# Optimization experiments

Hardware: AMD Instinct MI355X
Metric: run time of the kernel (lower is better)

The kernel has to match this reference:

```python
import jax, jax.numpy as jnp
import numpy as np

N_NODES = 50000
N_EDGES = 800000
IN_C, OUT_C, EDGE_F, HEADS, HID, FINAL = 8, 16, 8, 4, 64, 128
NEG_SLOPE = 0.2  # PyG GATConv default LeakyReLU slope


def setup_inputs() -> dict:
    key = jax.random.key(0)
    ks = jax.random.split(key, 12)
    s = 0.1
    return {
        "x": jax.random.normal(ks[0], (N_NODES, IN_C), jnp.float32),
        "edge_index": jax.random.randint(ks[1], (2, N_EDGES), 0, N_NODES, jnp.int64),
        "edge_attr": jax.random.normal(ks[2], (N_EDGES, EDGE_F), jnp.float32),
        # NNConv params: root weight, bias, edge-MLP Linear(EDGE_F -> IN_C*OUT_C)
        "ecc_root": jax.random.normal(ks[3], (IN_C, OUT_C), jnp.float32) * s,
        "ecc_bias": jnp.zeros((OUT_C,), jnp.float32),
        "mlp_w": jax.random.normal(ks[4], (EDGE_F, IN_C * OUT_C), jnp.float32) * s,
        "mlp_b": jnp.zeros((IN_C * OUT_C,), jnp.float32),
        # GATConv params
        "gat_lin": jax.random.normal(ks[5], (OUT_C, HEADS * HID), jnp.float32) * s,
        "att_src": jax.random.normal(ks[6], (HEADS, HID), jnp.float32) * s,
        "att_dst": jax.random.normal(ks[7], (HEADS, HID), jnp.float32) * s,
        "gat_bias": jnp.zeros((HEADS * HID,), jnp.float32),
        # final Linear
        "fc_w": jax.random.normal(ks[8], (HEADS * HID, FINAL), jnp.float32) * s,
        "fc_b": jnp.zeros((FINAL,), jnp.float32),
    }


def _forward(x, edge_index, edge_attr, ecc_root, ecc_bias, mlp_w, mlp_b,
             gat_lin, att_src, att_dst, gat_bias, fc_w, fc_b):
    src, dst = edge_index[0], edge_index[1]  # messages flow src -> dst

    # ---- NNConv (edge-conditioned conv), aggr='add' ----
    # per-edge weight matrices [E, IN_C, OUT_C] from edge MLP
    w_e = (edge_attr @ mlp_w + mlp_b).reshape(-1, IN_C, OUT_C)
    msg = jnp.einsum('ei,eio->eo', x[src], w_e)                 # [E, OUT_C]
    agg = jax.ops.segment_sum(msg, dst, num_segments=N_NODES)   # [N, OUT_C]
    h = jax.nn.relu(x @ ecc_root + agg + ecc_bias)              # [N, OUT_C]

    # ---- GATConv (heads concatenated) ----
    g = (h @ gat_lin).reshape(N_NODES, HEADS, HID)              # [N, H, D]
    a_src = jnp.einsum('nhd,hd->nh', g, att_src)                # [N, H]
    a_dst = jnp.einsum('nhd,hd->nh', g, att_dst)
    e = jax.nn.leaky_relu(a_src[src] + a_dst[dst], NEG_SLOPE)   # [E, H]
    # segment softmax over incoming edges of each dst node
    e_max = jax.ops.segment_max(e, dst, num_segments=N_NODES)   # [N, H]
    e_max = jnp.where(jnp.isfinite(e_max), e_max, 0.0)
    e_exp = jnp.exp(e - e_max[dst])                             # [E, H]
    denom = jax.ops.segment_sum(e_exp, dst, num_segments=N_NODES)
    alpha = e_exp / (denom[dst] + 1e-16)                        # [E, H]
    out = jax.ops.segment_sum(alpha[:, :, None] * g[src], dst,
                              num_segments=N_NODES)             # [N, H, D]
    out = jax.nn.relu(out.reshape(N_NODES, HEADS * HID) + gat_bias)

    # ---- final linear ----
    return out @ fc_w + fc_b                                    # [N, FINAL]


def reference(x, edge_index, edge_attr, ecc_root, ecc_bias, mlp_w, mlp_b,
              gat_lin, att_src, att_dst, gat_bias, fc_w, fc_b):
    return _forward(x, edge_index, edge_attr, ecc_root, ecc_bias, mlp_w, mlp_b,
                    gat_lin, att_src, att_dst, gat_bias, fc_w, fc_b)
```

## Files before the change

### kernel.cpp

```cpp
#include <hip/hip_runtime.h>
#include <hip/hip_fp16.h>

#define N_NODES 50000
#define N_EDGES 800000
#define IN_C 8
#define OUT_C 16
#define EDGE_F 8
#define HEADS 4
#define HID 64
#define GDIM (HEADS*HID)
#define FINAL 128
#define NEG_SLOPE 0.2f
#define EB ((N_EDGES+255)/256)
#define NBLK 196

__device__ __forceinline__ int clampn(int v) {
    return v < 0 ? 0 : (v >= N_NODES ? N_NODES - 1 : v);
}

__global__ __launch_bounds__(256) void k_histfold(
    const int* __restrict__ dst, int* __restrict__ cnt, int* __restrict__ rnk,
    const float* __restrict__ gat_lin,
    const float* __restrict__ att_src_w, const float* __restrict__ att_dst_w,
    float* __restrict__ wsrc, float* __restrict__ wdst)
{
    if (blockIdx.x < EB) {
        int e = blockIdx.x * 256 + threadIdx.x;
        if (e >= N_EDGES) return;
        rnk[e] = atomicAdd(&cnt[clampn(dst[e])], 1);
    } else {
        int t = threadIdx.x;
        if (t >= 64) return;
        int c = t >> 2, h = t & 3;
        float ws = 0.f, wd = 0.f;
        for (int k = 0; k < HID; k++) {
            float l = gat_lin[c * GDIM + h * HID + k];
            ws += l * att_src_w[h * HID + k];
            wd += l * att_dst_w[h * HID + k];
        }
        wsrc[t] = ws;
        wdst[t] = wd;
    }
}

__global__ __launch_bounds__(256) void k_part(const int* __restrict__ cnt,
                                              int* __restrict__ part)
{
    int i = blockIdx.x * 256 + threadIdx.x;
    int v = (i < N_NODES) ? cnt[i] : 0;
#pragma unroll
    for (int off = 32; off; off >>= 1) v += __shfl_down(v, off);
    __shared__ int ws[4];
    if ((threadIdx.x & 63) == 0) ws[threadIdx.x >> 6] = v;
    __syncthreads();
    if (threadIdx.x == 0) part[blockIdx.x] = ws[0] + ws[1] + ws[2] + ws[3];
}

__global__ __launch_bounds__(256) void k_scan1(const int* __restrict__ part,
                                               int* __restrict__ partscan)
{
    int t = threadIdx.x;
    int v = (t < NBLK) ? part[t] : 0;
    int lane = t & 63, wid = t >> 6;
    int incl = v;
#pragma unroll
    for (int off = 1; off < 64; off <<= 1) {
        int u = __shfl_up(incl, off);
        if (lane >= off) incl += u;
    }
    __shared__ int wsum[4];
    if (lane == 63) wsum[wid] = incl;
    __syncthreads();
    int add = 0;
    for (int w = 0; w < wid; w++) add += wsum[w];
    partscan[t] = incl - v + add;
}

__global__ __launch_bounds__(256) void k_add(const int* __restrict__ cnt,
                                             const int* __restrict__ partscan,
                                             int* __restrict__ offs)
{
    int i = blockIdx.x * 256 + threadIdx.x;
    int v = (i < N_NODES) ? cnt[i] : 0;
    int lane = threadIdx.x & 63, wid = threadIdx.x >> 6;
    int incl = v;
#pragma unroll
    for (int off = 1; off < 64; off <<= 1) {
        int u = __shfl_up(incl, off);
        if (lane >= off) incl += u;
    }
    __shared__ int wsum[4];
    if (lane == 63) wsum[wid] = incl;
    __syncthreads();
    int add = partscan[blockIdx.x];
    for (int w = 0; w < wid; w++) add += wsum[w];
    if (i < N_NODES) offs[i] = incl - v + add;
    if (i == 0) offs[N_NODES] = N_EDGES;
}

__global__ __launch_bounds__(256) void k_scatter(
    const int* __restrict__ src, const int* __restrict__ dst,
    const int* __restrict__ rnk, const int* __restrict__ offs,
    const float* __restrict__ ea,
    int2* __restrict__ se_csr, __half* __restrict__ ea_h)
{
    int e = blockIdx.x * 256 + threadIdx.x;
    if (e >= N_EDGES) return;
    int p = offs[clampn(dst[e])] + rnk[e];
    se_csr[p] = make_int2(clampn(src[e]), e);
    const float4* s4 = (const float4*)&ea[(size_t)e * EDGE_F];
    float4 lo = s4[0], hi = s4[1];
    __half2* d2 = (__half2*)&ea_h[(size_t)e * EDGE_F];
    d2[0] = __floats2half2_rn(lo.x, lo.y);
    d2[1] = __floats2half2_rn(lo.z, lo.w);
    d2[2] = __floats2half2_rn(hi.x, hi.y);
    d2[3] = __floats2half2_rn(hi.z, hi.w);
}

__global__ __launch_bounds__(256) void k2T_wave(
    const float* __restrict__ x,
    const int2* __restrict__ se_csr, const int* __restrict__ offs,
    const __half* __restrict__ ea_h,
    const float* __restrict__ mlp_w, const float* __restrict__ mlp_b,
    const float* __restrict__ ecc_root, const float* __restrict__ ecc_bias,
    const float* __restrict__ wsrc, const float* __restrict__ wdst,
    __half* __restrict__ h_tab, float* __restrict__ asrc, float* __restrict__ adst)
{
    __shared__ float smW[64 * 17];
    __shared__ float smb[128];
    __shared__ float sroot[128];
    __shared__ float sbias[16];
    __shared__ float sws[64], swd[64];
    __shared__ float sT[4][64];
    __shared__ float sxs[4][8];

    int t = threadIdx.x;
    for (int idx = t; idx < 1024; idx += 256)
        smW[(idx >> 4) * 17 + (idx & 15)] = mlp_w[idx];
    if (t < 128) smb[t] = mlp_b[t];
    if (t >= 128 && t < 256) sroot[t - 128] = ecc_root[t - 128];
    if (t < 16) sbias[t] = ecc_bias[t];
    if (t >= 32 && t < 96) sws[t - 32] = wsrc[t - 32];
    if (t >= 96 && t < 160) swd[t - 96] = wdst[t - 96];

    int wid = t >> 6, lane = t & 63;
    int n = blockIdx.x * 4 + wid;
    int f = lane >> 3, i = lane & 7;
    int beg = offs[n], end = offs[n + 1];

    float t0 = 0.f, t1 = 0.f, t2 = 0.f, t3 = 0.f, xs = 0.f;
    int j = beg;
    if (j + 3 < end) {
        int2 se0 = se_csr[j],     se1 = se_csr[j + 1];
        int2 se2 = se_csr[j + 2], se3 = se_csr[j + 3];
        float a0 = __half2float(ea_h[(unsigned)se0.y * EDGE_F + f]);
        float a1 = __half2float(ea_h[(unsigned)se1.y * EDGE_F + f]);
        float a2 = __half2float(ea_h[(unsigned)se2.y * EDGE_F + f]);
        float a3 = __half2float(ea_h[(unsigned)se3.y * EDGE_F + f]);
        float x0 = x[(unsigned)se0.x * IN_C + i];
        float x1 = x[(unsigned)se1.x * IN_C + i];
        float x2 = x[(unsigned)se2.x * IN_C + i];
        float x3 = x[(unsigned)se3.x * IN_C + i];
        j += 4;
        for (; j + 3 < end; j += 4) {
            int2 ne0 = se_csr[j],     ne1 = se_csr[j + 1];
            int2 ne2 = se_csr[j + 2], ne3 = se_csr[j + 3];
            float na0 = __half2float(ea_h[(unsigned)ne0.y * EDGE_F + f]);
            float na1 = __half2float(ea_h[(unsigned)ne1.y * EDGE_F + f]);
            float na2 = __half2float(ea_h[(unsigned)ne2.y * EDGE_F + f]);
            float na3 = __half2float(ea_h[(unsigned)ne3.y * EDGE_F + f]);
            float nx0 = x[(unsigned)ne0.x * IN_C + i];
            float nx1 = x[(unsigned)ne1.x * IN_C + i];
            float nx2 = x[(unsigned)ne2.x * IN_C + i];
            float nx3 = x[(unsigned)ne3.x * IN_C + i];
            t0 += a0 * x0; t1 += a1 * x1; t2 += a2 * x2; t3 += a3 * x3;
            xs += (x0 + x1) + (x2 + x3);
            a0 = na0; a1 = na1; a2 = na2; a3 = na3;
            x0 = nx0; x1 = nx1; x2 = nx2; x3 = nx3;
        }
        t0 += a0 * x0; t1 += a1 * x1; t2 += a2 * x2; t3 += a3 * x3;
        xs += (x0 + x1) + (x2 + x3);
    }
    for (; j < end; j++) {
        int2 se = se_csr[j];
        float a = __half2float(ea_h[(unsigned)se.y * EDGE_F + f]);
        float xv = x[(unsigned)se.x * IN_C + i];
        t0 += a * xv;
        xs += xv;
    }
    sT[wid][lane] = (t0 + t1) + (t2 + t3);
    if (f == 0) sxs[wid][i] = xs;
    __syncthreads();

    int o = lane & 15, p = lane >> 4;
    float v = 0.f;
#pragma unroll
    for (int q2 = 0; q2 < 16; q2++) {
        int jj = p * 16 + q2;
        v += smW[jj * 17 + o] * sT[wid][jj];
    }
    v += __shfl_down(v, 32);
    v += __shfl_down(v, 16);

    float hv = 0.f;
    if (lane < 16) {
        float vv = v + sbias[o];
#pragma unroll
        for (int ii = 0; ii < IN_C; ii++) {
            vv += smb[ii * 16 + o] * sxs[wid][ii];
            vv += x[n * IN_C + ii] * sroot[ii * 16 + o];
        }
        hv = fmaxf(vv, 0.f);
        h_tab[n * OUT_C + o] = __float2half_rn(hv);
    }
    float as = 0.f, ad = 0.f;
    int h2 = lane & 3;
#pragma unroll
    for (int c = 0; c < 16; c++) {
        float hc = __shfl(hv, c);
        as += hc * sws[c * 4 + h2];
        ad += hc * swd[c * 4 + h2];
    }
    if (lane < 4) {
        asrc[n * HEADS + lane] = as;
        adst[n * HEADS + lane] = ad;
    }
}

__global__ __launch_bounds__(256) void k_gatE(
    const int* __restrict__ offs, const int2* __restrict__ se_csr,
    const float* __restrict__ asrc, const float* __restrict__ adst,
    const __half* __restrict__ h_tab, float* __restrict__ U_all)
{
    int t = threadIdx.x;
    int wid = t >> 6, lane = t & 63;
    int n = blockIdx.x * 4 + wid;
    int h = lane >> 4, c = lane & 15;
    float adsth = adst[n * HEADS + h];
    int beg = offs[n], end = offs[n + 1];

    float U = 0.f, den = 0.f;
    int j = beg;
    if (j + 3 < end) {
        int s0 = se_csr[j].x,     s1 = se_csr[j + 1].x;
        int s2 = se_csr[j + 2].x, s3 = se_csr[j + 3].x;
        float av0 = asrc[(unsigned)s0 * HEADS + h], av1 = asrc[(unsigned)s1 * HEADS + h];
        float av2 = asrc[(unsigned)s2 * HEADS + h], av3 = asrc[(unsigned)s3 * HEADS + h];
        float h0 = __half2float(h_tab[(unsigned)s0 * OUT_C + c]);
        float h1 = __half2float(h_tab[(unsigned)s1 * OUT_C + c]);
        float h2v = __half2float(h_tab[(unsigned)s2 * OUT_C + c]);
        float h3v = __half2float(h_tab[(unsigned)s3 * OUT_C + c]);
        j += 4;
        for (; j + 3 < end; j += 4) {
            int ns0 = se_csr[j].x,     ns1 = se_csr[j + 1].x;
            int ns2 = se_csr[j + 2].x, ns3 = se_csr[j + 3].x;
            float nav0 = asrc[(unsigned)ns0 * HEADS + h];
            float nav1 = asrc[(unsigned)ns1 * HEADS + h];
            float nav2 = asrc[(unsigned)ns2 * HEADS + h];
            float nav3 = asrc[(unsigned)ns3 * HEADS + h];
            float nh0 = __half2float(h_tab[(unsigned)ns0 * OUT_C + c]);
            float nh1 = __half2float(h_tab[(unsigned)ns1 * OUT_C + c]);
            float nh2 = __half2float(h_tab[(unsigned)ns2 * OUT_C + c]);
            float nh3 = __half2float(h_tab[(unsigned)ns3 * OUT_C + c]);
            float v0 = av0 + adsth; v0 = v0 > 0.f ? v0 : NEG_SLOPE * v0;
            float v1 = av1 + adsth; v1 = v1 > 0.f ? v1 : NEG_SLOPE * v1;
            float v2 = av2 + adsth; v2 = v2 > 0.f ? v2 : NEG_SLOPE * v2;
            float v3 = av3 + adsth; v3 = v3 > 0.f ? v3 : NEG_SLOPE * v3;
            float p0 = __expf(v0), p1 = __expf(v1), p2 = __expf(v2), p3 = __expf(v3);
            den += (p0 + p1) + (p2 + p3);
            U += p0 * h0 + p1 * h1 + p2 * h2v + p3 * h3v;
            av0 = nav0; av1 = nav1; av2 = nav2; av3 = nav3;
            h0 = nh0; h1 = nh1; h2v = nh2; h3v = nh3;
        }
        float v0 = av0 + adsth; v0 = v0 > 0.f ? v0 : NEG_SLOPE * v0;
        float v1 = av1 + adsth; v1 = v1 > 0.f ? v1 : NEG_SLOPE * v1;
        float v2 = av2 + adsth; v2 = v2 > 0.f ? v2 : NEG_SLOPE * v2;
        float v3 = av3 + adsth; v3 = v3 > 0.f ? v3 : NEG_SLOPE * v3;
        float p0 = __expf(v0), p1 = __expf(v1), p2 = __expf(v2), p3 = __expf(v3);
        den += (p0 + p1) + (p2 + p3);
        U += p0 * h0 + p1 * h1 + p2 * h2v + p3 * h3v;
    }
    for (; j < end; j++) {
        int s = se_csr[j].x;
        float av = asrc[(unsigned)s * HEADS + h];
        float hvv = __half2float(h_tab[(unsigned)s * OUT_C + c]);
        float v = av + adsth; v = v > 0.f ? v : NEG_SLOPE * v;
        float pe = __expf(v);
        den += pe;
        U += pe * hvv;
    }
    U_all[(size_t)n * 64 + lane] = U / (den + 1e-16f);
}

#define FBM 64
__global__ __launch_bounds__(256) void k_fuse(
    const float* __restrict__ U_all, const float* __restrict__ gat_lin,
    const float* __restrict__ gat_bias, const float* __restrict__ fc_w,
    const float* __restrict__ fc_b, float* __restrict__ y)
{
    __shared__ float slin[16 * GDIM];
    __shared__ float sA[16][FBM + 4];
    __shared__ float sW[16][FINAL];
    int tid = threadIdx.x;
    int r0 = blockIdx.x * FBM;

    for (int idx = tid; idx < (16 * GDIM) / 4; idx += 256)
        ((float4*)slin)[idx] = ((const float4*)gat_lin)[idx];
    __syncthreads();

    int ar  = tid >> 2;
    int akq = (tid & 3) * 4;
    int grow = r0 + ar;

    int rg = tid >> 4;
    int cg = tid & 15;

    int skk = tid >> 4;
    int scc = (tid & 15) * 4;

    float acc[4][8];
#pragma unroll
    for (int r = 0; r < 4; r++)
#pragma unroll
        for (int c = 0; c < 8; c++) acc[r][c] = 0.f;

    for (int h = 0; h < HEADS; ++h) {
        float4 ua = make_float4(0.f, 0.f, 0.f, 0.f), ub = ua, uc4 = ua, ud = ua;
        if (grow < N_NODES) {
            const float4* up = (const float4*)&U_all[(size_t)grow * 64 + h * 16];
            ua = up[0]; ub = up[1]; uc4 = up[2]; ud = up[3];
        }
        float ureg[16] = {ua.x, ua.y, ua.z, ua.w,  ub.x, ub.y, ub.z, ub.w,
                          uc4.x, uc4.y, uc4.z, uc4.w,  ud.x, ud.y, ud.z, ud.w};

#pragma unroll
        for (int tt = 0; tt < 4; ++tt) {
            int k0 = h * 64 + tt * 16;
            float4 bv = *(const float4*)&gat_bias[k0 + akq];
            float g0 = 0.f, g1 = 0.f, g2 = 0.f, g3 = 0.f;
#pragma unroll
            for (int c = 0; c < 16; ++c) {
                float4 lv = *(const float4*)&slin[c * GDIM + k0 + akq];
                g0 += ureg[c] * lv.x;
                g1 += ureg[c] * lv.y;
                g2 += ureg[c] * lv.z;
                g3 += ureg[c] * lv.w;
            }
            __syncthreads();
            sA[akq + 0][ar] = fmaxf(g0 + bv.x, 0.f);
            sA[akq + 1][ar] = fmaxf(g1 + bv.y, 0.f);
            sA[akq + 2][ar] = fmaxf(g2 + bv.z, 0.f);
            sA[akq + 3][ar] = fmaxf(g3 + bv.w, 0.f);
            {
                const float* wrow = &fc_w[(size_t)(k0 + skk) * FINAL];
                *(float4*)&sW[skk][scc]      = *(const float4*)&wrow[scc];
                *(float4*)&sW[skk][scc + 64] = *(const float4*)&wrow[scc + 64];
            }
            __syncthreads();
#pragma unroll
            for (int kk = 0; kk < 16; ++kk) {
                float4 a  = *(const float4*)&sA[kk][rg * 4];
                float4 w0 = *(const float4*)&sW[kk][cg * 4];
                float4 w1 = *(const float4*)&sW[kk][cg * 4 + 64];
                float av[4] = {a.x, a.y, a.z, a.w};
#pragma unroll
                for (int r = 0; r < 4; r++) {
                    acc[r][0] += av[r] * w0.x;
                    acc[r][1] += av[r] * w0.y;
                    acc[r][2] += av[r] * w0.z;
                    acc[r][3] += av[r] * w0.w;
                    acc[r][4] += av[r] * w1.x;
                    acc[r][5] += av[r] * w1.y;
                    acc[r][6] += av[r] * w1.z;
                    acc[r][7] += av[r] * w1.w;
                }
            }
        }
    }

    float4 fb0 = *(const float4*)&fc_b[cg * 4];
    float4 fb1 = *(const float4*)&fc_b[cg * 4 + 64];
#pragma unroll
    for (int r = 0; r < 4; r++) {
        int row = r0 + rg * 4 + r;
        if (row < N_NODES) {
            float* yp = &y[(size_t)row * FINAL];
            *(float4*)&yp[cg * 4] =
                make_float4(acc[r][0] + fb0.x, acc[r][1] + fb0.y,
                            acc[r][2] + fb0.z, acc[r][3] + fb0.w);
            *(float4*)&yp[cg * 4 + 64] =
                make_float4(acc[r][4] + fb1.x, acc[r][5] + fb1.y,
                            acc[r][6] + fb1.z, acc[r][7] + fb1.w);
        }
    }
}

extern "C" void kernel_launch(void* const* d_in, const int* in_sizes, int n_in,
                              void* d_out, int out_size, void* d_ws, size_t ws_size,
                              hipStream_t stream)
{
    const float* x        = (const float*)d_in[0];
    const int*   ei       = (const int*)d_in[1];
    const float* ea       = (const float*)d_in[2];
    const float* ecc_root = (const float*)d_in[3];
    const float* ecc_bias = (const float*)d_in[4];
    const float* mlp_w    = (const float*)d_in[5];
    const float* mlp_b    = (const float*)d_in[6];
    const float* gat_lin  = (const float*)d_in[7];
    const float* att_src  = (const float*)d_in[8];
    const float* att_dst  = (const float*)d_in[9];
    const float* gat_bias = (const float*)d_in[10];
    const float* fc_w     = (const float*)d_in[11];
    const float* fc_b     = (const float*)d_in[12];
    float* y = (float*)d_out;

    const int* src = ei;
    const int* dst = ei + N_EDGES;

    float*  U_all = (float*)d_ws;
    float*  asrc  = U_all + (size_t)N_NODES * 64;
    float*  adst  = asrc + (size_t)N_NODES * HEADS;
    float*  wsrc  = adst + (size_t)N_NODES * HEADS;
    float*  wdst  = wsrc + 64;
    __half* ea_h  = (__half*)(wdst + 64);
    __half* h_tab = ea_h + (size_t)N_EDGES * EDGE_F;
    int*    cnt      = (int*)(h_tab + (size_t)N_NODES * OUT_C);
    int*    offs     = cnt + N_NODES;
    int*    part     = offs + N_NODES + 2;
    int*    partscan = part + 256;
    int*    rnk      = partscan + 256;
    int2*   se_csr   = (int2*)(rnk + N_EDGES);

    hipMemsetAsync(cnt, 0, sizeof(int) * N_NODES, stream);

    k_histfold<<<EB + 1, 256, 0, stream>>>(dst, cnt, rnk, gat_lin, att_src, att_dst,
                                           wsrc, wdst);
    k_part    <<<NBLK, 256, 0, stream>>>(cnt, part);
    k_scan1   <<<1, 256, 0, stream>>>(part, partscan);
    k_add     <<<NBLK, 256, 0, stream>>>(cnt, partscan, offs);
    k_scatter <<<EB, 256, 0, stream>>>(src, dst, rnk, offs, ea, se_csr, ea_h);

    k2T_wave  <<<N_NODES / 4, 256, 0, stream>>>(x, se_csr, offs, ea_h, mlp_w, mlp_b,
                                                ecc_root, ecc_bias, wsrc, wdst,
                                                h_tab, asrc, adst);
    k_gatE    <<<N_NODES / 4, 256, 0, stream>>>(offs, se_csr, asrc, adst, h_tab, U_all);
    k_fuse    <<<(N_NODES + FBM - 1) / FBM, 256, 0, stream>>>(U_all, gat_lin, gat_bias,
                                                              fc_w, fc_b, y);
}
```

Measured before the change: 313.8 us.

## Double-buffer shared tiles in fused GAT-output/FC kernel to halve barriers

The fused GAT projection plus final linear kernel now uses double-buffered shared memory for the activation tile and the fc_w tile. Each step computes and stages the next 16-wide k-slice while multiplying the current one, so it needs one barrier per step instead of two. The next head's U values are prefetched into registers a head ahead. In exchange, shared memory use and register pressure rise, which may lower occupancy.

```diff
diff --git a/kernel.cpp b/kernel.cpp
--- a/kernel.cpp
+++ b/kernel.cpp
@@ -299,14 +299,13 @@
     const float* __restrict__ fc_b, float* __restrict__ y)
 {
     __shared__ float slin[16 * GDIM];
-    __shared__ float sA[16][FBM + 4];
-    __shared__ float sW[16][FINAL];
+    __shared__ float sA[2][16][FBM + 4];
+    __shared__ float sW[2][16][FINAL];
     int tid = threadIdx.x;
     int r0 = blockIdx.x * FBM;
 
     for (int idx = tid; idx < (16 * GDIM) / 4; idx += 256)
         ((float4*)slin)[idx] = ((const float4*)gat_lin)[idx];
-    __syncthreads();
 
     int ar  = tid >> 2;
     int akq = (tid & 3) * 4;
@@ -324,58 +323,91 @@
 #pragma unroll
         for (int c = 0; c < 8; c++) acc[r][c] = 0.f;
 
+    const float4 z4 = make_float4(0.f, 0.f, 0.f, 0.f);
+    float4 cu0 = z4, cu1 = z4, cu2 = z4, cu3 = z4;
+    if (grow < N_NODES) {
+        const float4* up = (const float4*)&U_all[(size_t)grow * 64];
+        cu0 = up[0]; cu1 = up[1]; cu2 = up[2]; cu3 = up[3];
+    }
+
+#define GCOMP_WRITE(NB, K0N, U0, U1, U2, U3)                                   \
+    {                                                                          \
+        float4 bv = *(const float4*)&gat_bias[(K0N) + akq];                    \
+        float g0 = 0.f, g1 = 0.f, g2 = 0.f, g3 = 0.f;                          \
+        const float* lp0 = &slin[(K0N) + akq];                                 \
+        _Pragma("unroll")                                                      \
+        for (int q = 0; q < 4; ++q) {                                          \
+            float uq[4] = { q==0?U0.x:(q==1?U1.x:(q==2?U2.x:U3.x)),            \
+                            q==0?U0.y:(q==1?U1.y:(q==2?U2.y:U3.y)),            \
+                            q==0?U0.z:(q==1?U1.z:(q==2?U2.z:U3.z)),            \
+                            q==0?U0.w:(q==1?U1.w:(q==2?U2.w:U3.w)) };          \
+            _Pragma("unroll")                                                  \
+            for (int cc = 0; cc < 4; ++cc) {                                   \
+                float4 lv = *(const float4*)&lp0[(q * 4 + cc) * GDIM];         \
+                g0 += uq[cc] * lv.x;                                           \
+                g1 += uq[cc] * lv.y;                                           \
+                g2 += uq[cc] * lv.z;                                           \
+                g3 += uq[cc] * lv.w;                                           \
+            }                                                                  \
+        }                                                                      \
+        sA[NB][akq + 0][ar] = fmaxf(g0 + bv.x, 0.f);                           \
+        sA[NB][akq + 1][ar] = fmaxf(g1 + bv.y, 0.f);                           \
+        sA[NB][akq + 2][ar] = fmaxf(g2 + bv.z, 0.f);                           \
+        sA[NB][akq + 3][ar] = fmaxf(g3 + bv.w, 0.f);                           \
+    }
+
+#define WSTAGE(NB, K0N)                                                        \
+    {                                                                          \
+        const float* wrow = &fc_w[(size_t)((K0N) + skk) * FINAL];              \
+        *(float4*)&sW[NB][skk][scc]      = *(const float4*)&wrow[scc];         \
+        *(float4*)&sW[NB][skk][scc + 64] = *(const float4*)&wrow[scc + 64];    \
+    }
+
+#define MM(B)                                                                  \
+    _Pragma("unroll")                                                          \
+    for (int kk = 0; kk < 16; ++kk) {                                          \
+        float4 a  = *(const float4*)&sA[B][kk][rg * 4];                        \
+        float4 w0 = *(const float4*)&sW[B][kk][cg * 4];                        \
+        float4 w1 = *(const float4*)&sW[B][kk][cg * 4 + 64];                   \
+        float av[4] = {a.x, a.y, a.z, a.w};                                    \
+        _Pragma("unroll")                                                      \
+        for (int r = 0; r < 4; r++) {                                          \
+            acc[r][0] += av[r] * w0.x;                                         \
+            acc[r][1] += av[r] * w0.y;                                         \
+            acc[r][2] += av[r] * w0.z;                                         \
+            acc[r][3] += av[r] * w0.w;                                         \
+            acc[r][4] += av[r] * w1.x;                                         \
+            acc[r][5] += av[r] * w1.y;                                         \
+            acc[r][6] += av[r] * w1.z;                                         \
+            acc[r][7] += av[r] * w1.w;                                         \
+        }                                                                      \
+    }
+
+    __syncthreads();
+    GCOMP_WRITE(0, 0, cu0, cu1, cu2, cu3)
+    WSTAGE(0, 0)
+    __syncthreads();
+
     for (int h = 0; h < HEADS; ++h) {
-        float4 ua = make_float4(0.f, 0.f, 0.f, 0.f), ub = ua, uc4 = ua, ud = ua;
-        if (grow < N_NODES) {
-            const float4* up = (const float4*)&U_all[(size_t)grow * 64 + h * 16];
-            ua = up[0]; ub = up[1]; uc4 = up[2]; ud = up[3];
-        }
-        float ureg[16] = {ua.x, ua.y, ua.z, ua.w,  ub.x, ub.y, ub.z, ub.w,
-                          uc4.x, uc4.y, uc4.z, uc4.w,  ud.x, ud.y, ud.z, ud.w};
-
+        float4 nu0 = z4, nu1 = z4, nu2 = z4, nu3 = z4;
+        if (h < 3 && grow < N_NODES) {
+            const float4* up = (const float4*)&U_all[(size_t)grow * 64 + (h + 1) * 16];
+            nu0 = up[0]; nu1 = up[1]; nu2 = up[2]; nu3 = up[3];
+        }
 #pragma unroll
         for (int tt = 0; tt < 4; ++tt) {
             int k0 = h * 64 + tt * 16;
-            float4 bv = *(const float4*)&gat_bias[k0 + akq];
-            float g0 = 0.f, g1 = 0.f, g2 = 0.f, g3 = 0.f;
-#pragma unroll
-            for (int c = 0; c < 16; ++c) {
-                float4 lv = *(const float4*)&slin[c * GDIM + k0 + akq];
-                g0 += ureg[c] * lv.x;
-                g1 += ureg[c] * lv.y;
-                g2 += ureg[c] * lv.z;
-                g3 += ureg[c] * lv.w;
+            if (tt < 3) {
+                GCOMP_WRITE((tt + 1) & 1, k0 + 16, cu0, cu1, cu2, cu3)
+                WSTAGE((tt + 1) & 1, k0 + 16)
+            } else if (h < 3) {
+                GCOMP_WRITE(0, (h + 1) * 64, nu0, nu1, nu2, nu3)
+                WSTAGE(0, (h + 1) * 64)
             }
+            MM(tt & 1)
             __syncthreads();
-            sA[akq + 0][ar] = fmaxf(g0 + bv.x, 0.f);
-            sA[akq + 1][ar] = fmaxf(g1 + bv.y, 0.f);
-            sA[akq + 2][ar] = fmaxf(g2 + bv.z, 0.f);
-            sA[akq + 3][ar] = fmaxf(g3 + bv.w, 0.f);
-            {
-                const float* wrow = &fc_w[(size_t)(k0 + skk) * FINAL];
-                *(float4*)&sW[skk][scc]      = *(const float4*)&wrow[scc];
-                *(float4*)&sW[skk][scc + 64] = *(const float4*)&wrow[scc + 64];
-            }
-            __syncthreads();
-#pragma unroll
-            for (int kk = 0; kk < 16; ++kk) {
-                float4 a  = *(const float4*)&sA[kk][rg * 4];
-                float4 w0 = *(const float4*)&sW[kk][cg * 4];
-                float4 w1 = *(const float4*)&sW[kk][cg * 4 + 64];
-                float av[4] = {a.x, a.y, a.z, a.w};
-#pragma unroll
-                for (int r = 0; r < 4; r++) {
-                    acc[r][0] += av[r] * w0.x;
-                    acc[r][1] += av[r] * w0.y;
-                    acc[r][2] += av[r] * w0.z;
-                    acc[r][3] += av[r] * w0.w;
-                    acc[r][4] += av[r] * w1.x;
-                    acc[r][5] += av[r] * w1.y;
-                    acc[r][6] += av[r] * w1.z;
-                    acc[r][7] += av[r] * w1.w;
-                }
-            }
-        }
+        }
+        cu0 = nu0; cu1 = nu1; cu2 = nu2; cu3 = nu3;
     }
 
     float4 fb0 = *(const float4*)&fc_b[cg * 4];
@@ -393,6 +425,9 @@
                             acc[r][6] + fb1.z, acc[r][7] + fb1.w);
         }
     }
+#undef GCOMP_WRITE
+#undef WSTAGE
+#undef MM
 }
 
 extern "C" void kernel_launch(void* const* d_in, const int* in_sizes, int n_in,
```

Result: slower. 588.6 us (+87.6%).

## Double-buffer sA/sW tiles in k_fuse to halve barriers and overlap staging

Applied to the files above, without the earlier changes.

Splits the shared A and W tiles in the fused GAT-output/final-linear kernel into two buffers. Each step now computes the next 16-wide slice of the activation and stages the matching fc_w rows while running the matmul on the current buffer, so only one barrier is needed per tile instead of two. The next head's U values are prefetched into registers one head ahead. In exchange it doubles the shared memory used for the tiles and raises register pressure, which may reduce occupancy.

```diff
diff --git a/kernel.cpp b/kernel.cpp
--- a/kernel.cpp
+++ b/kernel.cpp
@@ -293,28 +293,73 @@
 }
 
 #define FBM 64
+
+#define GTERM(UC, CI)                                                          \
+    { float4 lv = *(const float4*)&lp0[(CI) * GDIM];                           \
+      g0 += (UC) * lv.x; g1 += (UC) * lv.y;                                    \
+      g2 += (UC) * lv.z; g3 += (UC) * lv.w; }
+
+#define GCOMP(NB, K0, U0, U1, U2, U3)                                          \
+    { float4 bv = *(const float4*)&gat_bias[(K0) + akq];                       \
+      const float* lp0 = &slin[(K0) + akq];                                    \
+      float g0 = 0.f, g1 = 0.f, g2 = 0.f, g3 = 0.f;                            \
+      GTERM((U0).x, 0)  GTERM((U0).y, 1)  GTERM((U0).z, 2)  GTERM((U0).w, 3)   \
+      GTERM((U1).x, 4)  GTERM((U1).y, 5)  GTERM((U1).z, 6)  GTERM((U1).w, 7)   \
+      GTERM((U2).x, 8)  GTERM((U2).y, 9)  GTERM((U2).z, 10) GTERM((U2).w, 11)  \
+      GTERM((U3).x, 12) GTERM((U3).y, 13) GTERM((U3).z, 14) GTERM((U3).w, 15)  \
+      sA[NB][akq + 0][ar] = fmaxf(g0 + bv.x, 0.f);                             \
+      sA[NB][akq + 1][ar] = fmaxf(g1 + bv.y, 0.f);                             \
+      sA[NB][akq + 2][ar] = fmaxf(g2 + bv.z, 0.f);                             \
+      sA[NB][akq + 3][ar] = fmaxf(g3 + bv.w, 0.f); }
+
+#define WSTAGE(NB, K0)                                                         \
+    { const float* wrow = &fc_w[(size_t)((K0) + skk) * FINAL];                 \
+      *(float4*)&sW[NB][skk][scc]      = *(const float4*)&wrow[scc];           \
+      *(float4*)&sW[NB][skk][scc + 64] = *(const float4*)&wrow[scc + 64]; }
+
+#define MMB(B)                                                                 \
+    { _Pragma("unroll")                                                        \
+      for (int kk = 0; kk < 16; ++kk) {                                        \
+        float4 a  = *(const float4*)&sA[B][kk][rg * 4];                        \
+        float4 w0 = *(const float4*)&sW[B][kk][cg * 4];                        \
+        float4 w1 = *(const float4*)&sW[B][kk][cg * 4 + 64];                   \
+        acc[0][0] += a.x * w0.x; acc[0][1] += a.x * w0.y;                      \
+        acc[0][2] += a.x * w0.z; acc[0][3] += a.x * w0.w;                      \
+        acc[0][4] += a.x * w1.x; acc[0][5] += a.x * w1.y;                      \
+        acc[0][6] += a.x * w1.z; acc[0][7] += a.x * w1.w;                      \
+        acc[1][0] += a.y * w0.x; acc[1][1] += a.y * w0.y;                      \
+        acc[1][2] += a.y * w0.z; acc[1][3] += a.y * w0.w;                      \
+        acc[1][4] += a.y * w1.x; acc[1][5] += a.y * w1.y;                      \
+        acc[1][6] += a.y * w1.z; acc[1][7] += a.y * w1.w;                      \
+        acc[2][0] += a.z * w0.x; acc[2][1] += a.z * w0.y;                      \
+        acc[2][2] += a.z * w0.z; acc[2][3] += a.z * w0.w;                      \
+        acc[2][4] += a.z * w1.x; acc[2][5] += a.z * w1.y;                      \
+        acc[2][6] += a.z * w1.z; acc[2][7] += a.z * w1.w;                      \
+        acc[3][0] += a.w * w0.x; acc[3][1] += a.w * w0.y;                      \
+        acc[3][2] += a.w * w0.z; acc[3][3] += a.w * w0.w;                      \
+        acc[3][4] += a.w * w1.x; acc[3][5] += a.w * w1.y;                      \
+        acc[3][6] += a.w * w1.z; acc[3][7] += a.w * w1.w;                      \
+      } }
+
 __global__ __launch_bounds__(256) void k_fuse(
     const float* __restrict__ U_all, const float* __restrict__ gat_lin,
     const float* __restrict__ gat_bias, const float* __restrict__ fc_w,
     const float* __restrict__ fc_b, float* __restrict__ y)
 {
     __shared__ float slin[16 * GDIM];
-    __shared__ float sA[16][FBM + 4];
-    __shared__ float sW[16][FINAL];
+    __shared__ float sA[2][16][FBM + 4];
+    __shared__ float sW[2][16][FINAL];
     int tid = threadIdx.x;
     int r0 = blockIdx.x * FBM;
 
     for (int idx = tid; idx < (16 * GDIM) / 4; idx += 256)
         ((float4*)slin)[idx] = ((const float4*)gat_lin)[idx];
-    __syncthreads();
 
     int ar  = tid >> 2;
     int akq = (tid & 3) * 4;
     int grow = r0 + ar;
-
     int rg = tid >> 4;
     int cg = tid & 15;
-
     int skk = tid >> 4;
     int scc = (tid & 15) * 4;
 
@@ -324,58 +369,45 @@
 #pragma unroll
         for (int c = 0; c < 8; c++) acc[r][c] = 0.f;
 
+    const float4 z4 = make_float4(0.f, 0.f, 0.f, 0.f);
+    float4 cu0 = z4, cu1 = z4, cu2 = z4, cu3 = z4;
+    float4 nu0 = z4, nu1 = z4, nu2 = z4, nu3 = z4;
+    if (grow < N_NODES) {
+        const float4* up = (const float4*)&U_all[(size_t)grow * 64];
+        cu0 = up[0]; cu1 = up[1]; cu2 = up[2]; cu3 = up[3];
+    }
+
+    __syncthreads();
+    GCOMP(0, 0, cu0, cu1, cu2, cu3)
+    WSTAGE(0, 0)
+    __syncthreads();
+
     for (int h = 0; h < HEADS; ++h) {
-        float4 ua = make_float4(0.f, 0.f, 0.f, 0.f), ub = ua, uc4 = ua, ud = ua;
-        if (grow < N_NODES) {
-            const float4* up = (const float4*)&U_all[(size_t)grow * 64 + h * 16];
-            ua = up[0]; ub = up[1]; uc4 = up[2]; ud = up[3];
-        }
-        float ureg[16] = {ua.x, ua.y, ua.z, ua.w,  ub.x, ub.y, ub.z, ub.w,
-                          uc4.x, uc4.y, uc4.z, uc4.w,  ud.x, ud.y, ud.z, ud.w};
-
-#pragma unroll
-        for (int tt = 0; tt < 4; ++tt) {
-            int k0 = h * 64 + tt * 16;
-            float4 bv = *(const float4*)&gat_bias[k0 + akq];
-            float g0 = 0.f, g1 = 0.f, g2 = 0.f, g3 = 0.f;
-#pragma unroll
-            for (int c = 0; c < 16; ++c) {
-                float4 lv = *(const float4*)&slin[c * GDIM + k0 + akq];
-                g0 += ureg[c] * lv.x;
-                g1 += ureg[c] * lv.y;
-                g2 += ureg[c] * lv.z;
-                g3 += ureg[c] * lv.w;
-            }
-            __syncthreads();
-            sA[akq + 0][ar] = fmaxf(g0 + bv.x, 0.f);
-            sA[akq + 1][ar] = fmaxf(g1 + bv.y, 0.f);
-            sA[akq + 2][ar] = fmaxf(g2 + bv.z, 0.f);
-            sA[akq + 3][ar] = fmaxf(g3 + bv.w, 0.f);
-            {
-                const float* wrow = &fc_w[(size_t)(k0 + skk) * FINAL];
-                *(float4*)&sW[skk][scc]      = *(const float4*)&wrow[scc];
-                *(float4*)&sW[skk][scc + 64] = *(const float4*)&wrow[scc + 64];
-            }
-            __syncthreads();
-#pragma unroll
-            for (int kk = 0; kk < 16; ++kk) {
-                float4 a  = *(const float4*)&sA[kk][rg * 4];
-                float4 w0 = *(const float4*)&sW[kk][cg * 4];
-                float4 w1 = *(const float4*)&sW[kk][cg * 4 + 64];
-                float av[4] = {a.x, a.y, a.z, a.w};
-#pragma unroll
-                for (int r = 0; r < 4; r++) {
-                    acc[r][0] += av[r] * w0.x;
-                    acc[r][1] += av[r] * w0.y;
-                    acc[r][2] += av[r] * w0.z;
-                    acc[r][3] += av[r] * w0.w;
-                    acc[r][4] += av[r] * w1.x;
-                    acc[r][5] += av[r] * w1.y;
-                    acc[r][6] += av[r] * w1.z;
-                    acc[r][7] += av[r] * w1.w;
-                }
-            }
-        }
+        int hb = h * 64;
+        nu0 = z4; nu1 = z4; nu2 = z4; nu3 = z4;
+        if (h < 3 && grow < N_NODES) {
+            const float4* up = (const float4*)&U_all[(size_t)grow * 64 + (h + 1) * 16];
+            nu0 = up[0]; nu1 = up[1]; nu2 = up[2]; nu3 = up[3];
+        }
+        GCOMP(1, hb + 16, cu0, cu1, cu2, cu3)
+        WSTAGE(1, hb + 16)
+        MMB(0)
+        __syncthreads();
+        GCOMP(0, hb + 32, cu0, cu1, cu2, cu3)
+        WSTAGE(0, hb + 32)
+        MMB(1)
+        __syncthreads();
+        GCOMP(1, hb + 48, cu0, cu1, cu2, cu3)
+        WSTAGE(1, hb + 48)
+        MMB(0)
+        __syncthreads();
+        if (h < 3) {
+            GCOMP(0, hb + 64, nu0, nu1, nu2, nu3)
+            WSTAGE(0, hb + 64)
+        }
+        MMB(1)
+        __syncthreads();
+        cu0 = nu0; cu1 = nu1; cu2 = nu2; cu3 = nu3;
     }
 
     float4 fb0 = *(const float4*)&fc_b[cg * 4];
```

After: 593.9 us. +89.3%, slower.
